# Kernel tuning notes

Measured on AMD Instinct MI355X. Metric: run time of the kernel, lower is better.

Reference implementation:

```python
import jax, jax.numpy as jnp
import numpy as np

N, L, E, H = 4, 4096, 1024, 1024


def setup_inputs() -> dict:
    key = jax.random.key(0)
    ks = jax.random.split(key, 7)
    s_in = 1.0 / np.sqrt(E)
    return {
        "X_embed": jax.random.normal(ks[0], (N, L, E), dtype=jnp.float32),
        "Wq": jax.random.normal(ks[1], (H, E), dtype=jnp.float32) * s_in,
        "bq": jnp.zeros((H,), dtype=jnp.float32),
        "Wk": jax.random.normal(ks[2], (H, E), dtype=jnp.float32) * s_in,
        "bk": jnp.zeros((H,), dtype=jnp.float32),
        "Wv": jax.random.normal(ks[3], (H, E), dtype=jnp.float32) * s_in,
        "bv": jnp.zeros((H,), dtype=jnp.float32),
    }


def reference(X_embed, Wq, bq, Wk, bk, Wv, bv):
    # Linear projections: (N, L, E) @ (E, H) + (H,) -> (N, L, H)
    Q = jnp.einsum('nle,he->nlh', X_embed, Wq) + bq
    K = jnp.einsum('nle,he->nlh', X_embed, Wk) + bk
    V = jnp.einsum('nle,he->nlh', X_embed, Wv) + bv
    # Scores (N, L, L); original scales by sqrt(Out.shape[2]) == sqrt(L)
    S = jnp.einsum('nah,nbh->nab', Q, K) / jnp.asarray(np.sqrt(float(L)), dtype=Q.dtype)
    # Original softmax is over dim=1 (the query axis 'a')
    A = jax.nn.softmax(S, axis=1)
    # 'nll,nlh->nlh': diagonal of A times V, elementwise over h
    diag = jnp.diagonal(A, axis1=1, axis2=2)  # (N, L)
    return diag[:, :, None] * V
```

## Files before the change

### kernel.cpp

```cpp
#include <hip/hip_runtime.h>
#include <hip/hip_bf16.h>
#include <stdint.h>

#define NB 4
#define LS 4096
#define ED 1024
#define HD 1024
#define MR (NB * LS)
#define SCALE_S (1.0f / 64.0f)

typedef __attribute__((ext_vector_type(8))) short bf16x8;
typedef __attribute__((ext_vector_type(8))) int   i32x8;
typedef __attribute__((ext_vector_type(4))) float f32x4;

__device__ __forceinline__ unsigned short f2bf(float f) {
    union { float f; uint32_t u; } x; x.f = f;
    uint32_t r = x.u + 0x7fffu + ((x.u >> 16) & 1u);
    return (unsigned short)(r >> 16);
}

__device__ __forceinline__ void load_lds16(const void* g, void* s) {
    __builtin_amdgcn_global_load_lds(
        (const __attribute__((address_space(1))) void*)g,
        (__attribute__((address_space(3))) void*)s, 16, 0, 0);
}

#define XCHUNKS (MR * ED / 4)
#define WCHUNKS (3 * ED * ED / 4)
__global__ void __launch_bounds__(256) cast_all_k(
    const float4* __restrict__ X, const float4* __restrict__ wq,
    const float4* __restrict__ wk, const float4* __restrict__ wv,
    ushort4* __restrict__ Xb, ushort4* __restrict__ Wall)
{
    const int i = blockIdx.x * 256 + threadIdx.x;
    if (i < XCHUNKS) {
        const float4 v = X[i];
        ushort4 o; o.x = f2bf(v.x); o.y = f2bf(v.y); o.z = f2bf(v.z); o.w = f2bf(v.w);
        Xb[i] = o;
    } else if (i < XCHUNKS + WCHUNKS) {
        const int j = i - XCHUNKS;
        const int s = j >> 18, jj = j & 0x3ffff;
        const float4 v = (s == 0 ? wq : s == 1 ? wk : wv)[jj];
        ushort4 o; o.x = f2bf(v.x); o.y = f2bf(v.y); o.z = f2bf(v.z); o.w = f2bf(v.w);
        Wall[j] = o;
    }
}

#define QK_BAR() do { asm volatile("" ::: "memory"); \
    __builtin_amdgcn_s_barrier(); asm volatile("" ::: "memory"); } while (0)
#define PH_MID() do { QK_BAR(); \
    asm volatile("s_waitcnt lgkmcnt(0)" ::: "memory"); \
    __builtin_amdgcn_sched_barrier(0); \
    __builtin_amdgcn_s_setprio(1); } while (0)
#define PH_END() do { __builtin_amdgcn_s_setprio(0); QK_BAR(); } while (0)
#define PH_END_VM6() do { __builtin_amdgcn_s_setprio(0); \
    asm volatile("s_waitcnt vmcnt(6)" ::: "memory"); QK_BAR(); } while (0)
#define PH_END_VM0() do { __builtin_amdgcn_s_setprio(0); \
    asm volatile("s_waitcnt vmcnt(0)" ::: "memory"); QK_BAR(); } while (0)

__device__ __forceinline__ void read_af(bf16x8 (&af)[4][2], const char* base,
                                        int arow, int sw7, int quad) {
#pragma unroll
    for (int mf = 0; mf < 4; mf++) {
        const char* r = base + (arow + mf * 16) * 128;
        af[mf][0] = *(const bf16x8*)(r + ((quad * 16) ^ sw7));
        af[mf][1] = *(const bf16x8*)(r + ((64 + quad * 16) ^ sw7));
    }
}
__device__ __forceinline__ void read_wf(bf16x8 (&wf)[4], const char* base,
                                        int wrow, int ks64, int sw7, int quad) {
#pragma unroll
    for (int nf = 0; nf < 4; nf++)
        wf[nf] = *(const bf16x8*)(base + (wrow + nf * 16) * 128 + ((ks64 + quad * 16) ^ sw7));
}
template<int KS>
__device__ __forceinline__ void mfma16(f32x4 (&acc)[4][4], const bf16x8 (&af)[4][2],
                                       const bf16x8 (&wf)[4]) {
#pragma unroll
    for (int mf = 0; mf < 4; mf++)
#pragma unroll
        for (int nf = 0; nf < 4; nf++)
            acc[mf][nf] = __builtin_amdgcn_mfma_f32_16x16x32_bf16(
                wf[nf], af[mf][KS], acc[mf][nf], 0, 0, 0);
}

__global__ void __launch_bounds__(512) __attribute__((amdgpu_waves_per_eu(2, 2)))
gemm_qk_fused8(const unsigned short* __restrict__ A,
               const unsigned short* __restrict__ W,
               const float* __restrict__ bq, const float* __restrict__ bk,
               unsigned char* __restrict__ Qf8t, unsigned char* __restrict__ Kf8t,
               float* __restrict__ diag)
{
    extern __shared__ char lds[];
    const int t = threadIdx.x;
    const int w = t >> 6, lane = t & 63, quad = lane >> 4, l16 = lane & 15;
    const int wm = w >> 1, wn = w & 1;

    const int swz = (blockIdx.x & 7) * 64 + (blockIdx.x >> 3);
    const long blockM = (long)(swz >> 3) * 256;
    const int  blockN = (swz & 7) * 128;

    const long srow = (long)(w * 8 + (lane >> 3)) * 2048
                    + (long)(((lane & 7) ^ (lane >> 3)) << 4);
    const char* gA  = (const char*)A + blockM * 2048 + srow;
    const char* gAh = gA + 128 * 2048;
    const char* gWq = (const char*)W + (long)blockN * 2048 + srow;
    const char* gWk = gWq + (long)1024 * 2048;
    char* dst = lds + w * 1024;

#define ST(G, OFF, KB) do { \
    load_lds16((G) + (KB), dst + (OFF)); \
    load_lds16((G) + 131072 + (KB), dst + (OFF) + 8192); } while (0)

    const char* A0 = lds;          const char* A1 = lds + 65536;
    const char* Q0 = lds + 32768;  const char* Q1 = lds + 65536 + 32768;
    const char* K0 = lds + 49152;  const char* K1 = lds + 65536 + 49152;

    const int arow = wm * 64 + l16;
    const int wrow = wn * 64 + l16;
    const int sw7  = (l16 & 7) << 4;

    f32x4 aq[4][4] = {}; f32x4 ak[4][4] = {};
    bf16x8 aF[4][2], wF[4];

    ST(gA, 0, 0); ST(gAh, 16384, 0); ST(gWq, 32768, 0); ST(gWk, 49152, 0);
    ST(gA, 65536, 128); ST(gAh, 65536 + 16384, 128); ST(gWq, 65536 + 32768, 128);
    asm volatile("s_waitcnt vmcnt(6)" ::: "memory");
    QK_BAR();

#pragma unroll 1
    for (int i = 0; i < 7; ++i) {
        const long k1 = (2L * i + 1) * 128, k2 = (2L * i + 2) * 128, k3 = (2L * i + 3) * 128;
        read_af(aF, A0, arow, sw7, quad);
        read_wf(wF, Q0, wrow, 0, sw7, quad);
        ST(gWk, 65536 + 49152, k1);
        asm volatile("s_waitcnt lgkmcnt(8)" ::: "memory");
        PH_MID(); mfma16<0>(aq, aF, wF); PH_END();
        read_wf(wF, Q0, wrow, 64, sw7, quad);
        ST(gA, 0, k2);
        PH_MID(); mfma16<1>(aq, aF, wF); PH_END();
        read_wf(wF, K0, wrow, 0, sw7, quad);
        ST(gAh, 16384, k2);
        PH_MID(); mfma16<0>(ak, aF, wF); PH_END();
        read_wf(wF, K0, wrow, 64, sw7, quad);
        ST(gWq, 32768, k2);
        PH_MID(); mfma16<1>(ak, aF, wF); PH_END_VM6();
        read_af(aF, A1, arow, sw7, quad);
        read_wf(wF, Q1, wrow, 0, sw7, quad);
        ST(gWk, 49152, k2);
        asm volatile("s_waitcnt lgkmcnt(8)" ::: "memory");
        PH_MID(); mfma16<0>(aq, aF, wF); PH_END();
        read_wf(wF, Q1, wrow, 64, sw7, quad);
        ST(gA, 65536, k3);
        PH_MID(); mfma16<1>(aq, aF, wF); PH_END();
        read_wf(wF, K1, wrow, 0, sw7, quad);
        ST(gAh, 65536 + 16384, k3);
        PH_MID(); mfma16<0>(ak, aF, wF); PH_END();
        read_wf(wF, K1, wrow, 64, sw7, quad);
        ST(gWq, 65536 + 32768, k3);
        PH_MID(); mfma16<1>(ak, aF, wF); PH_END_VM6();
    }
    {
        read_af(aF, A0, arow, sw7, quad);
        read_wf(wF, Q0, wrow, 0, sw7, quad);
        ST(gWk, 65536 + 49152, 15L * 128);
        asm volatile("s_waitcnt lgkmcnt(8)" ::: "memory");
        PH_MID(); mfma16<0>(aq, aF, wF); PH_END();
        read_wf(wF, Q0, wrow, 64, sw7, quad);
        PH_MID(); mfma16<1>(aq, aF, wF); PH_END();
        read_wf(wF, K0, wrow, 0, sw7, quad);
        PH_MID(); mfma16<0>(ak, aF, wF); PH_END();
        read_wf(wF, K0, wrow, 64, sw7, quad);
        PH_MID(); mfma16<1>(ak, aF, wF); PH_END_VM0();
        read_af(aF, A1, arow, sw7, quad);
        read_wf(wF, Q1, wrow, 0, sw7, quad);
        PH_MID(); mfma16<0>(aq, aF, wF); PH_END();
        read_wf(wF, Q1, wrow, 64, sw7, quad);
        PH_MID(); mfma16<1>(aq, aF, wF); PH_END();
        read_wf(wF, K1, wrow, 0, sw7, quad);
        PH_MID(); mfma16<0>(ak, aF, wF); PH_END();
        read_wf(wF, K1, wrow, 64, sw7, quad);
        PH_MID(); mfma16<1>(ak, aF, wF); PH_END();
    }
#undef ST

    float dp[4] = {0.f, 0.f, 0.f, 0.f};
#pragma unroll
    for (int nf = 0; nf < 4; nf++) {
        const int col = blockN + wn * 64 + nf * 16 + quad * 4;
        const float4 q4 = *(const float4*)(bq + col);
        const float4 k4 = *(const float4*)(bk + col);
#pragma unroll
        for (int mf = 0; mf < 4; mf++) {
            const size_t row = (size_t)(blockM + wm * 64 + mf * 16 + l16);
            const float vq0 = aq[mf][nf][0] + q4.x, vq1 = aq[mf][nf][1] + q4.y;
            const float vq2 = aq[mf][nf][2] + q4.z, vq3 = aq[mf][nf][3] + q4.w;
            const float vk0 = ak[mf][nf][0] + k4.x, vk1 = ak[mf][nf][1] + k4.y;
            const float vk2 = ak[mf][nf][2] + k4.z, vk3 = ak[mf][nf][3] + k4.w;
            uint32_t uq = 0, uk = 0;
            uq = __builtin_amdgcn_cvt_pk_fp8_f32(vq0, vq1, uq, false);
            uq = __builtin_amdgcn_cvt_pk_fp8_f32(vq2, vq3, uq, true);
            uk = __builtin_amdgcn_cvt_pk_fp8_f32(vk0, vk1, uk, false);
            uk = __builtin_amdgcn_cvt_pk_fp8_f32(vk2, vk3, uk, true);
            const size_t f8 = (row >> 4) * 16384 + (size_t)(col >> 4) * 256
                            + (row & 15) * 16 + (col & 15);
            *(uint32_t*)(Qf8t + f8) = uq;
            *(uint32_t*)(Kf8t + f8) = uk;
            dp[mf] += vq0 * vk0 + vq1 * vk1 + vq2 * vk2 + vq3 * vk3;
        }
    }
#pragma unroll
    for (int mf = 0; mf < 4; mf++) {
        float d = dp[mf];
        d += __shfl_xor(d, 16);
        d += __shfl_xor(d, 32);
        if (quad == 0)
            atomicAdd(&diag[blockM + wm * 64 + mf * 16 + l16], d);
    }
}

__device__ __forceinline__ void read_f8(i32x8 &f, const char* p) {
    const int4 lo = *(const int4*)p;
    const int4 hi = *(const int4*)(p + 256);
    f[0] = lo.x; f[1] = lo.y; f[2] = lo.z; f[3] = lo.w;
    f[4] = hi.x; f[5] = hi.y; f[6] = hi.z; f[7] = hi.w;
}

__global__ void __launch_bounds__(512)
gemm_f8_denomp(const unsigned char* __restrict__ Qt,
               const unsigned char* __restrict__ Kt,
               float* __restrict__ denom)
{
    extern __shared__ char lds[];
    const int t = threadIdx.x;
    const int w = t >> 6, lane = t & 63, quad = lane >> 4, l16 = lane & 15;
    const int wm = w >> 2, wn = w & 3;

    const int pos = (blockIdx.x & 7) * 256 + (blockIdx.x >> 3);
    const int z = pos >> 9;
    const int rem = pos & 511;
    const int blockM = (rem >> 4) * 128;
    const int blockN = (rem & 15) * 256;

    const size_t zoff = (size_t)z * LS * (size_t)HD;
    const long stg = (long)(t >> 7) * 16384 + (long)(t & 127) * 16;
    const unsigned char* gA = Qt + zoff + (size_t)(blockM >> 4) * 16384 + stg;
    const unsigned char* gB = Kt + zoff + (size_t)(blockN >> 4) * 16384 + stg;

#define DBUF(J) (lds + (J) * 49152)
#define DST(J, KT) do { \
    load_lds16(gA +          (long)(KT) * 2048, DBUF(J) +         w * 1024); \
    load_lds16(gA + 65536  + (long)(KT) * 2048, DBUF(J) + 8192  + w * 1024); \
    load_lds16(gB +          (long)(KT) * 2048, DBUF(J) + 16384 + w * 1024); \
    load_lds16(gB + 65536  + (long)(KT) * 2048, DBUF(J) + 24576 + w * 1024); \
    load_lds16(gB + 131072 + (long)(KT) * 2048, DBUF(J) + 32768 + w * 1024); \
    load_lds16(gB + 196608 + (long)(KT) * 2048, DBUF(J) + 40960 + w * 1024); } while (0)

    const int abase = (wm * 4) * 2048 + quad * 512 + l16 * 16;
    const int bbase = 16384 + (wn * 4) * 2048 + quad * 512 + l16 * 16;

    f32x4 acc[4][4] = {};
    i32x8 aF[4], bF[2];

#define DMFMA(NF, BI) \
    acc[mf][NF] = __builtin_amdgcn_mfma_scale_f32_16x16x128_f8f6f4( \
        aF[mf], bF[BI], acc[mf][NF], 0, 0, 0, 0x7f7f7f7f, 0, 0x7f7f7f7f)

#define DTILE(J, STG, ENDW) do { \
    const char* Db_ = DBUF(J); \
    read_f8(aF[0], Db_ + abase);        read_f8(aF[1], Db_ + abase + 2048); \
    read_f8(aF[2], Db_ + abase + 4096); read_f8(aF[3], Db_ + abase + 6144); \
    read_f8(bF[0], Db_ + bbase);        read_f8(bF[1], Db_ + bbase + 2048); \
    STG; \
    asm volatile("s_waitcnt lgkmcnt(0)" ::: "memory"); \
    __builtin_amdgcn_sched_barrier(0); \
    __builtin_amdgcn_s_setprio(1); \
    _Pragma("unroll") for (int mf = 0; mf < 4; mf++) { DMFMA(0, 0); DMFMA(1, 1); } \
    __builtin_amdgcn_s_setprio(0); \
    read_f8(bF[0], Db_ + bbase + 4096); read_f8(bF[1], Db_ + bbase + 6144); \
    asm volatile("s_waitcnt lgkmcnt(0)" ::: "memory"); \
    __builtin_amdgcn_sched_barrier(0); \
    __builtin_amdgcn_s_setprio(1); \
    _Pragma("unroll") for (int mf = 0; mf < 4; mf++) { DMFMA(2, 0); DMFMA(3, 1); } \
    __builtin_amdgcn_s_setprio(0); \
    ENDW; \
} while (0)

#define DEND6() do { asm volatile("s_waitcnt vmcnt(6)" ::: "memory"); QK_BAR(); } while (0)

    DST(0, 0); DST(1, 1);
    asm volatile("s_waitcnt vmcnt(6)" ::: "memory");
    QK_BAR();

#pragma unroll 1
    for (int i = 0; i < 2; ++i) {
        const int b = 3 * i;
        DTILE(0, DST(2, b + 2), DEND6());
        DTILE(1, DST(0, b + 3), DEND6());
        DTILE(2, DST(1, b + 4), DEND6());
    }
    DTILE(0, (void)0, { asm volatile("s_waitcnt vmcnt(0)" ::: "memory"); QK_BAR(); });
    DTILE(1, (void)0, (void)0);
#undef DBUF
#undef DST
#undef DMFMA
#undef DTILE
#undef DEND6

    float* dn = denom + (size_t)z * LS;
#pragma unroll
    for (int nf = 0; nf < 4; nf++) {
        float s = 0.f;
#pragma unroll
        for (int mf = 0; mf < 4; mf++)
#pragma unroll
            for (int r = 0; r < 4; r++)
                s += __expf(acc[mf][nf][r] * SCALE_S);
        s += __shfl_xor(s, 16);
        s += __shfl_xor(s, 32);
        if (quad == 0)
            atomicAdd(&dn[blockN + wn * 64 + nf * 16 + l16], s);
    }
}

__global__ void __launch_bounds__(512)
gemm_v8fin(const unsigned short* __restrict__ A,
           const unsigned short* __restrict__ Wv,
           const float* __restrict__ bv, const float* __restrict__ diag,
           const float* __restrict__ denom, float* __restrict__ out)
{
    extern __shared__ char lds[];
    const int t = threadIdx.x;
    const int w = t >> 6, lane = t & 63, quad = lane >> 4, l16 = lane & 15;
    const int wm = w >> 1, wn = w & 1;

    const int swz = (blockIdx.x & 7) * 64 + (blockIdx.x >> 3);
    const long blockM = (long)(swz >> 3) * 256;
    const int  blockN = (swz & 7) * 128;

    const int scol = (((t & 3) ^ ((t >> 2) & 3)) << 4);
    const char* gA0 = (const char*)A + (blockM + (t >> 2)) * 2048 + scol;
    const char* gA1 = gA0 + 128 * 2048;
    const char* gW0 = (const char*)Wv + ((long)blockN + (t >> 2)) * 2048 + scol;

    const int arow = wm * 64 + l16;
    const int wrow = wn * 64 + l16;
    const int rdoff = (quad * 16) ^ ((l16 & 3) << 4);

    f32x4 acc[4][4] = {};
    bf16x8 aF[4], wF[4];

#define VBA(J) (lds + (J) * 24576)
#define VST(J, KT) do { \
    load_lds16(gA0 + (long)(KT) * 64, VBA(J) + w * 1024); \
    load_lds16(gA1 + (long)(KT) * 64, VBA(J) + 8192 + w * 1024); \
    load_lds16(gW0 + (long)(KT) * 64, VBA(J) + 16384 + w * 1024); } while (0)
#define VREAD(J) do { \
    const char* Ab_ = VBA(J); const char* Wb_ = VBA(J) + 16384; \
    _Pragma("unroll") for (int mf = 0; mf < 4; mf++) \
        aF[mf] = *(const bf16x8*)(Ab_ + (arow + mf * 16) * 64 + rdoff); \
    _Pragma("unroll") for (int nf = 0; nf < 4; nf++) \
        wF[nf] = *(const bf16x8*)(Wb_ + (wrow + nf * 16) * 64 + rdoff); } while (0)
#define VCOMP() do { \
    asm volatile("s_waitcnt lgkmcnt(0)" ::: "memory"); \
    __builtin_amdgcn_sched_barrier(0); \
    __builtin_amdgcn_s_setprio(1); \
    _Pragma("unroll") for (int mf = 0; mf < 4; mf++) \
    _Pragma("unroll") for (int nf = 0; nf < 4; nf++) \
        acc[mf][nf] = __builtin_amdgcn_mfma_f32_16x16x32_bf16( \
            wF[nf], aF[mf], acc[mf][nf], 0, 0, 0); \
    __builtin_amdgcn_s_setprio(0); } while (0)
#define VEND3() do { asm volatile("s_waitcnt vmcnt(3)" ::: "memory"); QK_BAR(); } while (0)

    VST(0, 0); VST(1, 1);
    asm volatile("s_waitcnt vmcnt(3)" ::: "memory");
    QK_BAR();

#pragma unroll 1
    for (int i = 0; i < 10; ++i) {
        const int b = 3 * i;
        VREAD(0); VST(2, b + 2); VCOMP(); VEND3();
        VREAD(1); VST(0, b + 3); VCOMP(); VEND3();
        VREAD(2); VST(1, b + 4); VCOMP(); VEND3();
    }
    VREAD(0); VCOMP();
    asm volatile("s_waitcnt vmcnt(0)" ::: "memory"); QK_BAR();
    VREAD(1); VCOMP();
#undef VBA
#undef VST
#undef VREAD
#undef VCOMP
#undef VEND3

#pragma unroll
    for (int mf = 0; mf < 4; mf++) {
        const long row = blockM + wm * 64 + mf * 16 + l16;
        const float sc = __expf(diag[row] * SCALE_S) / denom[row];
#pragma unroll
        for (int nf = 0; nf < 4; nf++) {
            const int col = blockN + wn * 64 + nf * 16 + quad * 4;
            const float4 b4 = *(const float4*)(bv + col);
            float4 o;
            o.x = (acc[mf][nf][0] + b4.x) * sc;
            o.y = (acc[mf][nf][1] + b4.y) * sc;
            o.z = (acc[mf][nf][2] + b4.z) * sc;
            o.w = (acc[mf][nf][3] + b4.w) * sc;
            *(float4*)(out + row * 1024 + col) = o;
        }
    }
}

extern "C" void kernel_launch(void* const* d_in, const int* in_sizes, int n_in,
                              void* d_out, int out_size, void* d_ws, size_t ws_size,
                              hipStream_t stream)
{
    (void)in_sizes; (void)n_in; (void)out_size; (void)ws_size;
    const float* X  = (const float*)d_in[0];
    const float* Wq = (const float*)d_in[1];
    const float* bq = (const float*)d_in[2];
    const float* Wk = (const float*)d_in[3];
    const float* bk = (const float*)d_in[4];
    const float* Wv = (const float*)d_in[5];
    const float* bv = (const float*)d_in[6];
    float* out = (float*)d_out;

    char* p = (char*)d_ws;
    unsigned short* Xb   = (unsigned short*)p; p += (size_t)MR * ED * 2;
    unsigned short* Wall = (unsigned short*)p; p += (size_t)3072 * ED * 2;
    unsigned char*  Qf8t = (unsigned char*)p;  p += (size_t)MR * HD;
    unsigned char*  Kf8t = (unsigned char*)p;  p += (size_t)MR * HD;
    float* diag  = (float*)p; p += (size_t)MR * 4;
    float* denom = (float*)p; p += (size_t)MR * 4;

    dim3 blk(256);

    static int init8 = 0;
    if (!init8) {
        hipFuncSetAttribute((const void*)gemm_qk_fused8,
                            hipFuncAttributeMaxDynamicSharedMemorySize, 131072);
        hipFuncSetAttribute((const void*)gemm_f8_denomp,
                            hipFuncAttributeMaxDynamicSharedMemorySize, 147456);
        hipFuncSetAttribute((const void*)gemm_v8fin,
                            hipFuncAttributeMaxDynamicSharedMemorySize, 73728);
        init8 = 1;
    }

    cast_all_k<<<(XCHUNKS + WCHUNKS + 255) / 256, blk, 0, stream>>>(
        (const float4*)X, (const float4*)Wq, (const float4*)Wk, (const float4*)Wv,
        (ushort4*)Xb, (ushort4*)Wall);

    hipMemsetAsync(diag, 0, 2 * MR * sizeof(float), stream);

    gemm_qk_fused8<<<dim3(512), dim3(512), 131072, stream>>>(
        Xb, Wall, bq, bk, Qf8t, Kf8t, diag);

    gemm_f8_denomp<<<dim3(2048), dim3(512), 147456, stream>>>(Qf8t, Kf8t, denom);

    gemm_v8fin<<<dim3(512), dim3(512), 73728, stream>>>(
        Xb, Wall + (size_t)2048 * ED, bv, diag, denom, out);
}
```

Before: 331.3 us.

## Double-buffer FP8 denominator GEMM with split-phase B staging and plain grid

Replaces the triple-buffered LDS pipeline of the QK^T denominator GEMM with a double buffer (98 KB instead of 147 KB). Each k-tile is split into two MFMA phases, and the upper half of the B tile is prefetched separately so loads interleave at a finer grain, with vmcnt(4) waits. It also reassigns the B columns each wave reads, drops the XCD-aware block swizzle in favour of a plain 3D grid, and adjusts the atomic index to match. The smaller LDS footprint may allow more resident blocks, at the cost of shallower prefetch and possibly less L2 locality.

```diff
diff --git a/kernel.cpp b/kernel.cpp
--- a/kernel.cpp
+++ b/kernel.cpp
@@ -53,6 +53,8 @@
     __builtin_amdgcn_sched_barrier(0); \
     __builtin_amdgcn_s_setprio(1); } while (0)
 #define PH_END() do { __builtin_amdgcn_s_setprio(0); QK_BAR(); } while (0)
+#define PH_END_VM4() do { __builtin_amdgcn_s_setprio(0); \
+    asm volatile("s_waitcnt vmcnt(4)" ::: "memory"); QK_BAR(); } while (0)
 #define PH_END_VM6() do { __builtin_amdgcn_s_setprio(0); \
     asm volatile("s_waitcnt vmcnt(6)" ::: "memory"); QK_BAR(); } while (0)
 #define PH_END_VM0() do { __builtin_amdgcn_s_setprio(0); \
@@ -227,20 +229,18 @@
 }
 
 __global__ void __launch_bounds__(512)
-gemm_f8_denomp(const unsigned char* __restrict__ Qt,
-               const unsigned char* __restrict__ Kt,
-               float* __restrict__ denom)
+gemm_f8_den8w(const unsigned char* __restrict__ Qt,
+              const unsigned char* __restrict__ Kt,
+              float* __restrict__ denom)
 {
     extern __shared__ char lds[];
     const int t = threadIdx.x;
     const int w = t >> 6, lane = t & 63, quad = lane >> 4, l16 = lane & 15;
     const int wm = w >> 2, wn = w & 3;
 
-    const int pos = (blockIdx.x & 7) * 256 + (blockIdx.x >> 3);
-    const int z = pos >> 9;
-    const int rem = pos & 511;
-    const int blockM = (rem >> 4) * 128;
-    const int blockN = (rem & 15) * 256;
+    const int blockN = blockIdx.x * 256;
+    const int blockM = blockIdx.y * 128;
+    const int z = blockIdx.z;
 
     const size_t zoff = (size_t)z * LS * (size_t)HD;
     const long stg = (long)(t >> 7) * 16384 + (long)(t & 127) * 16;
@@ -248,64 +248,67 @@
     const unsigned char* gB = Kt + zoff + (size_t)(blockN >> 4) * 16384 + stg;
 
 #define DBUF(J) (lds + (J) * 49152)
-#define DST(J, KT) do { \
+#define DSTA(J, KT) do { \
     load_lds16(gA +          (long)(KT) * 2048, DBUF(J) +         w * 1024); \
-    load_lds16(gA + 65536  + (long)(KT) * 2048, DBUF(J) + 8192  + w * 1024); \
+    load_lds16(gA + 65536  + (long)(KT) * 2048, DBUF(J) + 8192  + w * 1024); } while (0)
+#define DSTBLO(J, KT) do { \
     load_lds16(gB +          (long)(KT) * 2048, DBUF(J) + 16384 + w * 1024); \
-    load_lds16(gB + 65536  + (long)(KT) * 2048, DBUF(J) + 24576 + w * 1024); \
+    load_lds16(gB + 65536  + (long)(KT) * 2048, DBUF(J) + 24576 + w * 1024); } while (0)
+#define DSTBHI(J, KT) do { \
     load_lds16(gB + 131072 + (long)(KT) * 2048, DBUF(J) + 32768 + w * 1024); \
     load_lds16(gB + 196608 + (long)(KT) * 2048, DBUF(J) + 40960 + w * 1024); } while (0)
 
     const int abase = (wm * 4) * 2048 + quad * 512 + l16 * 16;
-    const int bbase = 16384 + (wn * 4) * 2048 + quad * 512 + l16 * 16;
+    const int bbase = 16384 + wn * 2048 + quad * 512 + l16 * 16;
 
     f32x4 acc[4][4] = {};
     i32x8 aF[4], bF[2];
 
-#define DMFMA(NF, BI) \
-    acc[mf][NF] = __builtin_amdgcn_mfma_scale_f32_16x16x128_f8f6f4( \
-        aF[mf], bF[BI], acc[mf][NF], 0, 0, 0, 0x7f7f7f7f, 0, 0x7f7f7f7f)
-
-#define DTILE(J, STG, ENDW) do { \
+#define DMFMA2(NF0, NF1) do { \
+    _Pragma("unroll") for (int mf = 0; mf < 4; mf++) { \
+        acc[mf][NF0] = __builtin_amdgcn_mfma_scale_f32_16x16x128_f8f6f4( \
+            aF[mf], bF[0], acc[mf][NF0], 0, 0, 0, 0x7f7f7f7f, 0, 0x7f7f7f7f); \
+        acc[mf][NF1] = __builtin_amdgcn_mfma_scale_f32_16x16x128_f8f6f4( \
+            aF[mf], bF[1], acc[mf][NF1], 0, 0, 0, 0x7f7f7f7f, 0, 0x7f7f7f7f); } } while (0)
+
+#define DPHA(J, STG, K) do { \
     const char* Db_ = DBUF(J); \
     read_f8(aF[0], Db_ + abase);        read_f8(aF[1], Db_ + abase + 2048); \
     read_f8(aF[2], Db_ + abase + 4096); read_f8(aF[3], Db_ + abase + 6144); \
-    read_f8(bF[0], Db_ + bbase);        read_f8(bF[1], Db_ + bbase + 2048); \
+    read_f8(bF[0], Db_ + bbase);        read_f8(bF[1], Db_ + bbase + 8192); \
     STG; \
-    asm volatile("s_waitcnt lgkmcnt(0)" ::: "memory"); \
-    __builtin_amdgcn_sched_barrier(0); \
-    __builtin_amdgcn_s_setprio(1); \
-    _Pragma("unroll") for (int mf = 0; mf < 4; mf++) { DMFMA(0, 0); DMFMA(1, 1); } \
-    __builtin_amdgcn_s_setprio(0); \
-    read_f8(bF[0], Db_ + bbase + 4096); read_f8(bF[1], Db_ + bbase + 6144); \
-    asm volatile("s_waitcnt lgkmcnt(0)" ::: "memory"); \
-    __builtin_amdgcn_sched_barrier(0); \
-    __builtin_amdgcn_s_setprio(1); \
-    _Pragma("unroll") for (int mf = 0; mf < 4; mf++) { DMFMA(2, 0); DMFMA(3, 1); } \
-    __builtin_amdgcn_s_setprio(0); \
-    ENDW; \
-} while (0)
-
-#define DEND6() do { asm volatile("s_waitcnt vmcnt(6)" ::: "memory"); QK_BAR(); } while (0)
-
-    DST(0, 0); DST(1, 1);
-    asm volatile("s_waitcnt vmcnt(6)" ::: "memory");
+    asm volatile("s_waitcnt lgkmcnt(8)" ::: "memory"); \
+    PH_MID(); DMFMA2(0, 1); PH_END(); } while (0)
+#define DPHB(J, STG, ENDW) do { \
+    const char* Db_ = DBUF(J); \
+    read_f8(bF[0], Db_ + bbase + 16384); read_f8(bF[1], Db_ + bbase + 24576); \
+    STG; \
+    PH_MID(); DMFMA2(2, 3); ENDW; } while (0)
+
+    DSTA(0, 0); DSTBLO(0, 0); DSTBHI(0, 0);
+    DSTA(1, 1); DSTBLO(1, 1);
+    asm volatile("s_waitcnt vmcnt(4)" ::: "memory");
     QK_BAR();
 
 #pragma unroll 1
-    for (int i = 0; i < 2; ++i) {
-        const int b = 3 * i;
-        DTILE(0, DST(2, b + 2), DEND6());
-        DTILE(1, DST(0, b + 3), DEND6());
-        DTILE(2, DST(1, b + 4), DEND6());
-    }
-    DTILE(0, (void)0, { asm volatile("s_waitcnt vmcnt(0)" ::: "memory"); QK_BAR(); });
-    DTILE(1, (void)0, (void)0);
+    for (int i = 0; i < 3; ++i) {
+        const int k1 = 2 * i + 1, k2 = 2 * i + 2, k3 = 2 * i + 3;
+        DPHA(0, DSTBHI(1, k1), k1);
+        DPHB(0, { DSTA(0, k2); DSTBLO(0, k2); }, PH_END_VM4());
+        DPHA(1, DSTBHI(0, k2), k2);
+        DPHB(1, { DSTA(1, k3); DSTBLO(1, k3); }, PH_END_VM4());
+    }
+    DPHA(0, DSTBHI(1, 7), 7);
+    DPHB(0, (void)0, PH_END_VM0());
+    DPHA(1, (void)0, 7);
+    DPHB(1, (void)0, { __builtin_amdgcn_s_setprio(0); });
 #undef DBUF
-#undef DST
-#undef DMFMA
-#undef DTILE
-#undef DEND6
+#undef DSTA
+#undef DSTBLO
+#undef DSTBHI
+#undef DMFMA2
+#undef DPHA
+#undef DPHB
 
     float* dn = denom + (size_t)z * LS;
 #pragma unroll
@@ -319,7 +322,7 @@
         s += __shfl_xor(s, 16);
         s += __shfl_xor(s, 32);
         if (quad == 0)
-            atomicAdd(&dn[blockN + wn * 64 + nf * 16 + l16], s);
+            atomicAdd(&dn[blockN + (nf * 4 + wn) * 16 + l16], s);
     }
 }
 
@@ -438,8 +441,8 @@
     if (!init8) {
         hipFuncSetAttribute((const void*)gemm_qk_fused8,
                             hipFuncAttributeMaxDynamicSharedMemorySize, 131072);
-        hipFuncSetAttribute((const void*)gemm_f8_denomp,
-                            hipFuncAttributeMaxDynamicSharedMemorySize, 147456);
+        hipFuncSetAttribute((const void*)gemm_f8_den8w,
+                            hipFuncAttributeMaxDynamicSharedMemorySize, 98304);
         hipFuncSetAttribute((const void*)gemm_v8fin,
                             hipFuncAttributeMaxDynamicSharedMemorySize, 73728);
         init8 = 1;
@@ -454,7 +457,7 @@
     gemm_qk_fused8<<<dim3(512), dim3(512), 131072, stream>>>(
         Xb, Wall, bq, bk, Qf8t, Kf8t, diag);
 
-    gemm_f8_denomp<<<dim3(2048), dim3(512), 147456, stream>>>(Qf8t, Kf8t, denom);
+    gemm_f8_den8w<<<dim3(16, 32, 4), dim3(512), 98304, stream>>>(Qf8t, Kf8t, denom);
 
     gemm_v8fin<<<dim3(512), dim3(512), 73728, stream>>>(
         Xb, Wall + (size_t)2048 * ED, bv, diag, denom, out);
```

New measurement: 354.6 us. 1.07x slower.
